# Performance work log

Measured on AMD Instinct MI355X. Metric: run time of the kernel, lower is better.

## Reference

```python
import jax, jax.numpy as jnp
import numpy as np

D_MODEL = 768
NUM_HEADS = 12
D_K = D_MODEL // NUM_HEADS


def setup_inputs() -> dict:
    key = jax.random.key(0)
    ks = jax.random.split(key, 11)
    B, S = 2, 2048
    s = 1.0 / np.sqrt(D_MODEL)
    inp = {
        'q': jax.random.normal(ks[0], (B, S, D_MODEL), jnp.float32),
        'k': jax.random.normal(ks[1], (B, S, D_MODEL), jnp.float32),
        'v': jax.random.normal(ks[2], (B, S, D_MODEL), jnp.float32),
        'w_q': jax.random.normal(ks[3], (D_MODEL, D_MODEL), jnp.float32) * s,
        'b_q': jnp.zeros((D_MODEL,), jnp.float32),
        'w_k': jax.random.normal(ks[4], (D_MODEL, D_MODEL), jnp.float32) * s,
        'b_k': jnp.zeros((D_MODEL,), jnp.float32),
        'w_v': jax.random.normal(ks[5], (D_MODEL, D_MODEL), jnp.float32) * s,
        'b_v': jnp.zeros((D_MODEL,), jnp.float32),
        'w_o': jax.random.normal(ks[6], (D_MODEL, D_MODEL), jnp.float32) * s,
        'b_o': jnp.zeros((D_MODEL,), jnp.float32),
    }
    return inp


def _split_heads(x):
    # (B, S, D) -> (B, H, S, d_k)
    B, S, _ = x.shape
    return x.reshape(B, S, NUM_HEADS, D_K).transpose(0, 2, 1, 3)


def reference(q, k, v, w_q, b_q, w_k, b_k, w_v, b_v, w_o, b_o):
    qh = _split_heads(q @ w_q + b_q)
    kh = _split_heads(k @ w_k + b_k)
    vh = _split_heads(v @ w_v + b_v)
    scale = 1.0 / jnp.sqrt(jnp.asarray(D_K, qh.dtype))
    scores = jnp.einsum('bhqd,bhkd->bhqk', qh, kh) * scale  # [B,H,Sq,Sk]
    attn_weights = jax.nn.softmax(scores, axis=-1)
    ctx = jnp.einsum('bhqk,bhkd->bhqd', attn_weights, vh)
    B, H, S, _ = ctx.shape
    ctx = ctx.transpose(0, 2, 1, 3).reshape(B, S, D_MODEL)
    out = ctx @ w_o + b_o  # dropout = identity (eval mode)
    return out, attn_weights
```

## Files before the change

### kernel.cpp

```cpp
#include <hip/hip_runtime.h>
#include <math.h>

#define HH 12
#define SS 2048
#define DM 768
#define DK 64

typedef _Float16 f16x8 __attribute__((ext_vector_type(8)));
typedef _Float16 f16x4 __attribute__((ext_vector_type(4)));
typedef float    f32x4 __attribute__((ext_vector_type(4)));

#define MFMA_F16(A, B, C) __builtin_amdgcn_mfma_f32_16x16x32_f16((A), (B), (C), 0, 0, 0)

template <int MODE>
__global__ __launch_bounds__(256) void gemm_bias_kernel(
        const float* __restrict__ A, const float* __restrict__ W,
        const float* __restrict__ bias, float* __restrict__ C,
        _Float16* __restrict__ Chi, _Float16* __restrict__ Clo)
{
    __shared__ float Ast[16][68];
    __shared__ float Bs[16][68];

    const int tid = threadIdx.x;
    const int tx = tid & 15, ty = tid >> 4;
    const int n0 = blockIdx.x * 64;
    const int m0 = blockIdx.y * 64;

    float acc[4][4] = {};

    for (int kt = 0; kt < 48; ++kt) {
        __syncthreads();
        #pragma unroll
        for (int it = 0; it < 4; ++it) {
            int idx = tid + it * 256;
            int r = idx >> 4, c = idx & 15;
            Ast[c][r] = A[(size_t)(m0 + r) * DM + kt * 16 + c];
        }
        {
            int r = tid >> 4, c = tid & 15;
            *(float4*)&Bs[r][c << 2] =
                *(const float4*)&W[(size_t)(kt * 16 + r) * DM + n0 + (c << 2)];
        }
        __syncthreads();

        #pragma unroll 4
        for (int kk = 0; kk < 16; ++kk) {
            float4 a4 = *(const float4*)&Ast[kk][ty << 2];
            float4 b4 = *(const float4*)&Bs[kk][tx << 2];
            float av[4] = {a4.x, a4.y, a4.z, a4.w};
            float bv[4] = {b4.x, b4.y, b4.z, b4.w};
            #pragma unroll
            for (int i = 0; i < 4; ++i)
                #pragma unroll
                for (int j = 0; j < 4; ++j)
                    acc[i][j] = fmaf(av[i], bv[j], acc[i][j]);
        }
    }

    const float4 bb4 = *(const float4*)&bias[n0 + (tx << 2)];
    const float bvv[4] = {bb4.x, bb4.y, bb4.z, bb4.w};

    if (MODE == 0) {
        #pragma unroll
        for (int i = 0; i < 4; ++i) {
            int m = m0 + ty * 4 + i;
            float4 o;
            o.x = acc[i][0] + bvv[0];
            o.y = acc[i][1] + bvv[1];
            o.z = acc[i][2] + bvv[2];
            o.w = acc[i][3] + bvv[3];
            *(float4*)&C[(size_t)m * DM + n0 + (tx << 2)] = o;
        }
    } else if (MODE == 1) {
        const int h = blockIdx.x;
        #pragma unroll
        for (int i = 0; i < 4; ++i) {
            int m = m0 + ty * 4 + i;
            int b_ = m >> 11, s_ = m & 2047;
            size_t base = (((size_t)(b_ * HH + h) * SS + s_) << 6) + (tx << 2);
            f16x4 hi, lo;
            #pragma unroll
            for (int j = 0; j < 4; ++j) {
                float v = acc[i][j] + bvv[j];
                _Float16 hv = (_Float16)v;
                hi[j] = hv;
                lo[j] = (_Float16)(v - (float)hv);
            }
            *(f16x4*)&Chi[base] = hi;
            *(f16x4*)&Clo[base] = lo;
        }
    } else {
        const int h  = blockIdx.x;
        const int m  = m0 + ty * 4;
        const int b_ = m >> 11;
        const int s_ = m & 2047;
        #pragma unroll
        for (int j = 0; j < 4; ++j) {
            int dk = (tx << 2) + j;
            size_t base = ((size_t)(b_ * HH + h) * DK + dk) * SS + s_;
            f16x4 hi, lo;
            #pragma unroll
            for (int i = 0; i < 4; ++i) {
                float v = acc[i][j] + bvv[j];
                _Float16 hv = (_Float16)v;
                hi[i] = hv;
                lo[i] = (_Float16)(v - (float)hv);
            }
            *(f16x4*)&Chi[base] = hi;
            *(f16x4*)&Clo[base] = lo;
        }
    }
}

__global__ __launch_bounds__(256) void attn_kernel(
        const _Float16* __restrict__ Qhi, const _Float16* __restrict__ Qlo,
        const _Float16* __restrict__ Khi, const _Float16* __restrict__ Klo,
        const _Float16* __restrict__ Vthi, const _Float16* __restrict__ Vtlo,
        float* __restrict__ attnW, float* __restrict__ ctx)
{
    __shared__ float Ps[4][16][34];

    const int tid  = threadIdx.x;
    const int wave = tid >> 6;
    const int lane = tid & 63;
    const int lrow = lane & 15;
    const int lk   = (lane >> 4) * 8;
    const int grow = (lane >> 4) * 4;

    const int qt = blockIdx.x;
    const int bh = blockIdx.y;
    const int qw0 = qt * 64 + wave * 16;
    const size_t qkbase = (size_t)bh * SS * DK;
    const size_t vbase  = (size_t)bh * DK * SS;

    f16x8 qhi[2], qlo[2];
    {
        const size_t qidx = qkbase + (size_t)(qw0 + lrow) * DK + lk;
        qhi[0] = *(const f16x8*)&Qhi[qidx];
        qhi[1] = *(const f16x8*)&Qhi[qidx + 32];
        qlo[0] = *(const f16x8*)&Qlo[qidx];
        qlo[1] = *(const f16x8*)&Qlo[qidx + 32];
    }

    float lsum[4] = {0.f, 0.f, 0.f, 0.f};
    #pragma unroll 2
    for (int kt = 0; kt < 128; ++kt) {
        const size_t kidx = qkbase + (size_t)(kt * 16 + lrow) * DK + lk;
        f16x8 khi0 = *(const f16x8*)&Khi[kidx];
        f16x8 khi1 = *(const f16x8*)&Khi[kidx + 32];
        f16x8 klo0 = *(const f16x8*)&Klo[kidx];
        f16x8 klo1 = *(const f16x8*)&Klo[kidx + 32];
        f32x4 acc = {0.f, 0.f, 0.f, 0.f};
        acc = MFMA_F16(qhi[0], khi0, acc);
        acc = MFMA_F16(qhi[1], khi1, acc);
        acc = MFMA_F16(qlo[0], khi0, acc);
        acc = MFMA_F16(qlo[1], khi1, acc);
        acc = MFMA_F16(qhi[0], klo0, acc);
        acc = MFMA_F16(qhi[1], klo1, acc);
        #pragma unroll
        for (int r = 0; r < 4; ++r)
            lsum[r] += __expf(acc[r] * 0.125f);
    }

    #pragma unroll
    for (int r = 0; r < 4; ++r) {
        lsum[r] += __shfl_xor(lsum[r], 1, 64);
        lsum[r] += __shfl_xor(lsum[r], 2, 64);
        lsum[r] += __shfl_xor(lsum[r], 4, 64);
        lsum[r] += __shfl_xor(lsum[r], 8, 64);
    }
    float rl[4];
    #pragma unroll
    for (int r = 0; r < 4; ++r) rl[r] = 1.0f / lsum[r];

    f32x4 Oacc[4];
    #pragma unroll
    for (int n = 0; n < 4; ++n) Oacc[n] = (f32x4){0.f, 0.f, 0.f, 0.f};

    float (*ps)[34] = Ps[wave];

    for (int kt = 0; kt < 64; ++kt) {
        #pragma unroll
        for (int sub = 0; sub < 2; ++sub) {
            const int k16 = kt * 2 + sub;
            const size_t kidx = qkbase + (size_t)(k16 * 16 + lrow) * DK + lk;
            f16x8 khi0 = *(const f16x8*)&Khi[kidx];
            f16x8 khi1 = *(const f16x8*)&Khi[kidx + 32];
            f16x8 klo0 = *(const f16x8*)&Klo[kidx];
            f16x8 klo1 = *(const f16x8*)&Klo[kidx + 32];
            f32x4 acc = {0.f, 0.f, 0.f, 0.f};
            acc = MFMA_F16(qhi[0], khi0, acc);
            acc = MFMA_F16(qhi[1], khi1, acc);
            acc = MFMA_F16(qlo[0], khi0, acc);
            acc = MFMA_F16(qlo[1], khi1, acc);
            acc = MFMA_F16(qhi[0], klo0, acc);
            acc = MFMA_F16(qhi[1], klo1, acc);
            #pragma unroll
            for (int r = 0; r < 4; ++r) {
                float p = __expf(acc[r] * 0.125f) * rl[r];
                attnW[((size_t)bh * SS + qw0 + grow + r) * SS + k16 * 16 + lrow] = p;
                ps[grow + r][sub * 16 + lrow] = p * 512.0f;
            }
        }
        float pf[8];
        #pragma unroll
        for (int j = 0; j < 8; ++j) pf[j] = ps[lrow][lk + j];
        f16x8 phi, plo;
        #pragma unroll
        for (int j = 0; j < 8; ++j) {
            _Float16 h = (_Float16)pf[j];
            phi[j] = h;
            plo[j] = (_Float16)(pf[j] - (float)h);
        }
        #pragma unroll
        for (int n = 0; n < 4; ++n) {
            const size_t vidx = vbase + (size_t)(n * 16 + lrow) * SS + kt * 32 + lk;
            f16x8 vhi = *(const f16x8*)&Vthi[vidx];
            f16x8 vlo = *(const f16x8*)&Vtlo[vidx];
            Oacc[n] = MFMA_F16(phi, vhi, Oacc[n]);
            Oacc[n] = MFMA_F16(plo, vhi, Oacc[n]);
            Oacc[n] = MFMA_F16(phi, vlo, Oacc[n]);
        }
    }

    const int b_ = bh / HH, h_ = bh % HH;
    #pragma unroll
    for (int n = 0; n < 4; ++n)
        #pragma unroll
        for (int r = 0; r < 4; ++r) {
            int q = qw0 + grow + r;
            ctx[((size_t)b_ * SS + q) * DM + h_ * DK + n * 16 + lrow] =
                Oacc[n][r] * 0.001953125f;
        }
}

extern "C" void kernel_launch(void* const* d_in, const int* in_sizes, int n_in,
                              void* d_out, int out_size, void* d_ws, size_t ws_size,
                              hipStream_t stream) {
    const float* q   = (const float*)d_in[0];
    const float* k   = (const float*)d_in[1];
    const float* v   = (const float*)d_in[2];
    const float* w_q = (const float*)d_in[3];
    const float* b_q = (const float*)d_in[4];
    const float* w_k = (const float*)d_in[5];
    const float* b_k = (const float*)d_in[6];
    const float* w_v = (const float*)d_in[7];
    const float* b_v = (const float*)d_in[8];
    const float* w_o = (const float*)d_in[9];
    const float* b_o = (const float*)d_in[10];

    float* out   = (float*)d_out;
    float* attnW = out + (size_t)2 * SS * DM;

    _Float16* wsh  = (_Float16*)d_ws;
    const size_t PL = (size_t)2 * HH * SS * DK;
    _Float16* Qhi  = wsh;
    _Float16* Qlo  = wsh + PL;
    _Float16* Khi  = wsh + 2 * PL;
    _Float16* Klo  = wsh + 3 * PL;
    _Float16* Vthi = wsh + 4 * PL;
    _Float16* Vtlo = wsh + 5 * PL;
    float* ctx     = (float*)(wsh + 6 * PL);

    dim3 gg(12, 64), blk(256);
    gemm_bias_kernel<1><<<gg, blk, 0, stream>>>(q, w_q, b_q, nullptr, Qhi, Qlo);
    gemm_bias_kernel<1><<<gg, blk, 0, stream>>>(k, w_k, b_k, nullptr, Khi, Klo);
    gemm_bias_kernel<2><<<gg, blk, 0, stream>>>(v, w_v, b_v, nullptr, Vthi, Vtlo);

    attn_kernel<<<dim3(32, 24), blk, 0, stream>>>(Qhi, Qlo, Khi, Klo, Vthi, Vtlo,
                                                  attnW, ctx);

    gemm_bias_kernel<0><<<gg, blk, 0, stream>>>(ctx, w_o, b_o, out, nullptr, nullptr);
}
```

Before: 1.236 ms.

## Use split-fp16 MFMA projection GEMMs and single-pass attention with deferred normalization

The fp32 FMA projection GEMMs are replaced by MFMA GEMMs on split hi/lo fp16 operands. Weights are pre-converted and transposed into scratch space inside the output buffers, and the V output is transposed through LDS so stores are coalesced. The attention kernel drops its separate row-sum pass. It writes unnormalized exp scores, then rescales the attention-weight rows afterwards and normalizes ctx by the row sum, trading the second QK^T recomputation for an extra read/write of attnW. Unnormalized exp without max subtraction risks overflow, and the output needs an extra copy kernel because the out buffer is reused as scratch.

New measurement: 1.317 ms. 6.5% more time.

```diff
diff --git a/kernel.cpp b/kernel.cpp
--- a/kernel.cpp
+++ b/kernel.cpp
@@ -12,103 +12,144 @@
 
 #define MFMA_F16(A, B, C) __builtin_amdgcn_mfma_f32_16x16x32_f16((A), (B), (C), 0, 0, 0)
 
+__global__ __launch_bounds__(256) void conv_w_kernel(
+        const float* __restrict__ w0, const float* __restrict__ w1,
+        const float* __restrict__ w2, const float* __restrict__ w3,
+        _Float16* hi0, _Float16* lo0, _Float16* hi1, _Float16* lo1,
+        _Float16* hi2, _Float16* lo2, _Float16* hi3, _Float16* lo3)
+{
+    __shared__ float T[64][68];
+    const int z = blockIdx.z;
+    const float* W = (z == 0) ? w0 : (z == 1) ? w1 : (z == 2) ? w2 : w3;
+    _Float16* Whi  = (z == 0) ? hi0 : (z == 1) ? hi1 : (z == 2) ? hi2 : hi3;
+    _Float16* Wlo  = (z == 0) ? lo0 : (z == 1) ? lo1 : (z == 2) ? lo2 : lo3;
+
+    const int tid = threadIdx.x;
+    const int k0 = blockIdx.y * 64, n0 = blockIdx.x * 64;
+
+    #pragma unroll
+    for (int i = 0; i < 4; ++i) {
+        int r = (tid >> 4) + i * 16;
+        int c = (tid & 15) * 4;
+        *(float4*)&T[r][c] = *(const float4*)&W[(size_t)(k0 + r) * DM + n0 + c];
+    }
+    __syncthreads();
+
+    const int n = tid >> 2, kq = (tid & 3) * 16;
+    f16x8 ha, la, hb, lb;
+    #pragma unroll
+    for (int j = 0; j < 8; ++j) {
+        float v = T[kq + j][n];
+        _Float16 h = (_Float16)v;
+        ha[j] = h; la[j] = (_Float16)(v - (float)h);
+    }
+    #pragma unroll
+    for (int j = 0; j < 8; ++j) {
+        float v = T[kq + 8 + j][n];
+        _Float16 h = (_Float16)v;
+        hb[j] = h; lb[j] = (_Float16)(v - (float)h);
+    }
+    size_t o = (size_t)(n0 + n) * DM + k0 + kq;
+    *(f16x8*)&Whi[o]     = ha;
+    *(f16x8*)&Whi[o + 8] = hb;
+    *(f16x8*)&Wlo[o]     = la;
+    *(f16x8*)&Wlo[o + 8] = lb;
+}
+
 template <int MODE>
-__global__ __launch_bounds__(256) void gemm_bias_kernel(
-        const float* __restrict__ A, const float* __restrict__ W,
-        const float* __restrict__ bias, float* __restrict__ C,
-        _Float16* __restrict__ Chi, _Float16* __restrict__ Clo)
+__global__ __launch_bounds__(256) void gemm16_kernel(
+        const float* __restrict__ A, const _Float16* __restrict__ Bhi,
+        const _Float16* __restrict__ Blo, const float* __restrict__ bias,
+        _Float16* __restrict__ Chi, _Float16* __restrict__ Clo,
+        float* __restrict__ Cf)
 {
-    __shared__ float Ast[16][68];
-    __shared__ float Bs[16][68];
-
-    const int tid = threadIdx.x;
-    const int tx = tid & 15, ty = tid >> 4;
-    const int n0 = blockIdx.x * 64;
-    const int m0 = blockIdx.y * 64;
-
-    float acc[4][4] = {};
-
-    for (int kt = 0; kt < 48; ++kt) {
+    const int tid  = threadIdx.x;
+    const int wave = tid >> 6, lane = tid & 63;
+    const int lrow = lane & 15;
+    const int lk   = (lane >> 4) * 8;
+    const int grow = (lane >> 4) * 4;
+    const int n0   = blockIdx.x * 64;
+    const int m0   = blockIdx.y * 64;
+    const int mr   = m0 + wave * 16 + lrow;
+
+    f32x4 acc[4];
+    #pragma unroll
+    for (int nf = 0; nf < 4; ++nf) acc[nf] = (f32x4){0.f, 0.f, 0.f, 0.f};
+
+    const float* Arow = A + (size_t)mr * DM;
+
+    #pragma unroll 2
+    for (int kt = 0; kt < 24; ++kt) {
+        const int k0 = kt * 32 + lk;
+        float4 x = *(const float4*)&Arow[k0];
+        float4 y = *(const float4*)&Arow[k0 + 4];
+        float vv[8] = {x.x, x.y, x.z, x.w, y.x, y.y, y.z, y.w};
+        f16x8 ah, al;
+        #pragma unroll
+        for (int j = 0; j < 8; ++j) {
+            _Float16 h = (_Float16)vv[j];
+            ah[j] = h; al[j] = (_Float16)(vv[j] - (float)h);
+        }
+        #pragma unroll
+        for (int nf = 0; nf < 4; ++nf) {
+            const size_t bo = (size_t)(n0 + nf * 16 + lrow) * DM + k0;
+            f16x8 bh_ = *(const f16x8*)&Bhi[bo];
+            f16x8 bl_ = *(const f16x8*)&Blo[bo];
+            acc[nf] = MFMA_F16(ah, bh_, acc[nf]);
+            acc[nf] = MFMA_F16(al, bh_, acc[nf]);
+            acc[nf] = MFMA_F16(ah, bl_, acc[nf]);
+        }
+    }
+
+    float bb[4];
+    #pragma unroll
+    for (int nf = 0; nf < 4; ++nf) bb[nf] = bias[n0 + nf * 16 + lrow];
+
+    if (MODE == 0) {
+        const int h = blockIdx.x;
+        #pragma unroll
+        for (int nf = 0; nf < 4; ++nf)
+            #pragma unroll
+            for (int r = 0; r < 4; ++r) {
+                int m = m0 + wave * 16 + grow + r;
+                int b_ = m >> 11, s_ = m & 2047;
+                float v = acc[nf][r] + bb[nf];
+                _Float16 h16 = (_Float16)v;
+                size_t o = (((size_t)(b_ * HH + h) * SS + s_) << 6) + nf * 16 + lrow;
+                Chi[o] = h16;
+                Clo[o] = (_Float16)(v - (float)h16);
+            }
+    } else if (MODE == 1) {
+        __shared__ _Float16 T[2][64][72];
+        #pragma unroll
+        for (int nf = 0; nf < 4; ++nf)
+            #pragma unroll
+            for (int r = 0; r < 4; ++r) {
+                float v = acc[nf][r] + bb[nf];
+                _Float16 h16 = (_Float16)v;
+                int ml = wave * 16 + grow + r;
+                T[0][nf * 16 + lrow][ml] = h16;
+                T[1][nf * 16 + lrow][ml] = (_Float16)(v - (float)h16);
+            }
         __syncthreads();
-        #pragma unroll
-        for (int it = 0; it < 4; ++it) {
-            int idx = tid + it * 256;
-            int r = idx >> 4, c = idx & 15;
-            Ast[c][r] = A[(size_t)(m0 + r) * DM + kt * 16 + c];
-        }
-        {
-            int r = tid >> 4, c = tid & 15;
-            *(float4*)&Bs[r][c << 2] =
-                *(const float4*)&W[(size_t)(kt * 16 + r) * DM + n0 + (c << 2)];
-        }
-        __syncthreads();
-
-        #pragma unroll 4
-        for (int kk = 0; kk < 16; ++kk) {
-            float4 a4 = *(const float4*)&Ast[kk][ty << 2];
-            float4 b4 = *(const float4*)&Bs[kk][tx << 2];
-            float av[4] = {a4.x, a4.y, a4.z, a4.w};
-            float bv[4] = {b4.x, b4.y, b4.z, b4.w};
+        const int h  = blockIdx.x;
+        const int b_ = m0 >> 11, s0 = m0 & 2047;
+        int row = tid >> 1;
+        int p = row >> 6, dk = row & 63, sh = (tid & 1) * 32;
+        const _Float16* src = &T[p][dk][sh];
+        _Float16* dst = (p ? Clo : Chi) +
+                        ((size_t)(b_ * HH + h) * DK + dk) * SS + s0 + sh;
+        #pragma unroll
+        for (int j = 0; j < 32; j += 8)
+            *(f16x8*)&dst[j] = *(const f16x8*)&src[j];
+    } else {
+        #pragma unroll
+        for (int nf = 0; nf < 4; ++nf)
             #pragma unroll
-            for (int i = 0; i < 4; ++i)
-                #pragma unroll
-                for (int j = 0; j < 4; ++j)
-                    acc[i][j] = fmaf(av[i], bv[j], acc[i][j]);
-        }
-    }
-
-    const float4 bb4 = *(const float4*)&bias[n0 + (tx << 2)];
-    const float bvv[4] = {bb4.x, bb4.y, bb4.z, bb4.w};
-
-    if (MODE == 0) {
-        #pragma unroll
-        for (int i = 0; i < 4; ++i) {
-            int m = m0 + ty * 4 + i;
-            float4 o;
-            o.x = acc[i][0] + bvv[0];
-            o.y = acc[i][1] + bvv[1];
-            o.z = acc[i][2] + bvv[2];
-            o.w = acc[i][3] + bvv[3];
-            *(float4*)&C[(size_t)m * DM + n0 + (tx << 2)] = o;
-        }
-    } else if (MODE == 1) {
-        const int h = blockIdx.x;
-        #pragma unroll
-        for (int i = 0; i < 4; ++i) {
-            int m = m0 + ty * 4 + i;
-            int b_ = m >> 11, s_ = m & 2047;
-            size_t base = (((size_t)(b_ * HH + h) * SS + s_) << 6) + (tx << 2);
-            f16x4 hi, lo;
-            #pragma unroll
-            for (int j = 0; j < 4; ++j) {
-                float v = acc[i][j] + bvv[j];
-                _Float16 hv = (_Float16)v;
-                hi[j] = hv;
-                lo[j] = (_Float16)(v - (float)hv);
+            for (int r = 0; r < 4; ++r) {
+                int m = m0 + wave * 16 + grow + r;
+                Cf[(size_t)m * DM + n0 + nf * 16 + lrow] = acc[nf][r] + bb[nf];
             }
-            *(f16x4*)&Chi[base] = hi;
-            *(f16x4*)&Clo[base] = lo;
-        }
-    } else {
-        const int h  = blockIdx.x;
-        const int m  = m0 + ty * 4;
-        const int b_ = m >> 11;
-        const int s_ = m & 2047;
-        #pragma unroll
-        for (int j = 0; j < 4; ++j) {
-            int dk = (tx << 2) + j;
-            size_t base = ((size_t)(b_ * HH + h) * DK + dk) * SS + s_;
-            f16x4 hi, lo;
-            #pragma unroll
-            for (int i = 0; i < 4; ++i) {
-                float v = acc[i][j] + bvv[j];
-                _Float16 hv = (_Float16)v;
-                hi[i] = hv;
-                lo[i] = (_Float16)(v - (float)hv);
-            }
-            *(f16x4*)&Chi[base] = hi;
-            *(f16x4*)&Clo[base] = lo;
-        }
     }
 }
 
@@ -143,36 +184,6 @@
     }
 
     float lsum[4] = {0.f, 0.f, 0.f, 0.f};
-    #pragma unroll 2
-    for (int kt = 0; kt < 128; ++kt) {
-        const size_t kidx = qkbase + (size_t)(kt * 16 + lrow) * DK + lk;
-        f16x8 khi0 = *(const f16x8*)&Khi[kidx];
-        f16x8 khi1 = *(const f16x8*)&Khi[kidx + 32];
-        f16x8 klo0 = *(const f16x8*)&Klo[kidx];
-        f16x8 klo1 = *(const f16x8*)&Klo[kidx + 32];
-        f32x4 acc = {0.f, 0.f, 0.f, 0.f};
-        acc = MFMA_F16(qhi[0], khi0, acc);
-        acc = MFMA_F16(qhi[1], khi1, acc);
-        acc = MFMA_F16(qlo[0], khi0, acc);
-        acc = MFMA_F16(qlo[1], khi1, acc);
-        acc = MFMA_F16(qhi[0], klo0, acc);
-        acc = MFMA_F16(qhi[1], klo1, acc);
-        #pragma unroll
-        for (int r = 0; r < 4; ++r)
-            lsum[r] += __expf(acc[r] * 0.125f);
-    }
-
-    #pragma unroll
-    for (int r = 0; r < 4; ++r) {
-        lsum[r] += __shfl_xor(lsum[r], 1, 64);
-        lsum[r] += __shfl_xor(lsum[r], 2, 64);
-        lsum[r] += __shfl_xor(lsum[r], 4, 64);
-        lsum[r] += __shfl_xor(lsum[r], 8, 64);
-    }
-    float rl[4];
-    #pragma unroll
-    for (int r = 0; r < 4; ++r) rl[r] = 1.0f / lsum[r];
-
     f32x4 Oacc[4];
     #pragma unroll
     for (int n = 0; n < 4; ++n) Oacc[n] = (f32x4){0.f, 0.f, 0.f, 0.f};
@@ -188,18 +199,20 @@
             f16x8 khi1 = *(const f16x8*)&Khi[kidx + 32];
             f16x8 klo0 = *(const f16x8*)&Klo[kidx];
             f16x8 klo1 = *(const f16x8*)&Klo[kidx + 32];
-            f32x4 acc = {0.f, 0.f, 0.f, 0.f};
-            acc = MFMA_F16(qhi[0], khi0, acc);
-            acc = MFMA_F16(qhi[1], khi1, acc);
-            acc = MFMA_F16(qlo[0], khi0, acc);
-            acc = MFMA_F16(qlo[1], khi1, acc);
-            acc = MFMA_F16(qhi[0], klo0, acc);
-            acc = MFMA_F16(qhi[1], klo1, acc);
+            f32x4 cA = {0.f, 0.f, 0.f, 0.f};
+            f32x4 cB = {0.f, 0.f, 0.f, 0.f};
+            cA = MFMA_F16(qhi[0], khi0, cA);
+            cA = MFMA_F16(qhi[1], khi1, cA);
+            cA = MFMA_F16(qlo[0], khi0, cA);
+            cB = MFMA_F16(qlo[1], khi1, cB);
+            cB = MFMA_F16(qhi[0], klo0, cB);
+            cB = MFMA_F16(qhi[1], klo1, cB);
             #pragma unroll
             for (int r = 0; r < 4; ++r) {
-                float p = __expf(acc[r] * 0.125f) * rl[r];
-                attnW[((size_t)bh * SS + qw0 + grow + r) * SS + k16 * 16 + lrow] = p;
-                ps[grow + r][sub * 16 + lrow] = p * 512.0f;
+                float pv = __expf((cA[r] + cB[r]) * 0.125f);
+                lsum[r] += pv;
+                attnW[((size_t)bh * SS + qw0 + grow + r) * SS + k16 * 16 + lrow] = pv;
+                ps[grow + r][sub * 16 + lrow] = pv * 16.0f;
             }
         }
         float pf[8];
@@ -223,6 +236,33 @@
         }
     }
 
+    #pragma unroll
+    for (int r = 0; r < 4; ++r) {
+        lsum[r] += __shfl_xor(lsum[r], 1, 64);
+        lsum[r] += __shfl_xor(lsum[r], 2, 64);
+        lsum[r] += __shfl_xor(lsum[r], 4, 64);
+        lsum[r] += __shfl_xor(lsum[r], 8, 64);
+    }
+    float rl[4];
+    #pragma unroll
+    for (int r = 0; r < 4; ++r) rl[r] = 1.0f / lsum[r];
+
+    if (lrow == 0) {
+        #pragma unroll
+        for (int r = 0; r < 4; ++r) ps[grow + r][32] = rl[r];
+    }
+
+    for (int r16 = 0; r16 < 16; ++r16) {
+        float mrl = ps[r16][32];
+        float4* row4 = (float4*)&attnW[((size_t)bh * SS + qw0 + r16) * SS];
+        #pragma unroll
+        for (int it = 0; it < 8; ++it) {
+            float4 vv = row4[it * 64 + lane];
+            vv.x *= mrl; vv.y *= mrl; vv.z *= mrl; vv.w *= mrl;
+            row4[it * 64 + lane] = vv;
+        }
+    }
+
     const int b_ = bh / HH, h_ = bh % HH;
     #pragma unroll
     for (int n = 0; n < 4; ++n)
@@ -230,8 +270,19 @@
         for (int r = 0; r < 4; ++r) {
             int q = qw0 + grow + r;
             ctx[((size_t)b_ * SS + q) * DM + h_ * DK + n * 16 + lrow] =
-                Oacc[n][r] * 0.001953125f;
-        }
+                Oacc[n][r] * rl[r] * 0.0625f;
+        }
+}
+
+__global__ __launch_bounds__(256) void copy_kernel(
+        float* __restrict__ dst, const float* __restrict__ src)
+{
+    const size_t total4 = (size_t)2 * SS * DM / 4;
+    size_t i = (size_t)blockIdx.x * 256 + threadIdx.x;
+    const size_t stride = (size_t)gridDim.x * 256;
+    float4* d4 = (float4*)dst;
+    const float4* s4 = (const float4*)src;
+    for (; i < total4; i += stride) d4[i] = s4[i];
 }
 
 extern "C" void kernel_launch(void* const* d_in, const int* in_sizes, int n_in,
@@ -252,7 +303,7 @@
     float* out   = (float*)d_out;
     float* attnW = out + (size_t)2 * SS * DM;
 
-    _Float16* wsh  = (_Float16*)d_ws;
+    _Float16* wsh = (_Float16*)d_ws;
     const size_t PL = (size_t)2 * HH * SS * DK;
     _Float16* Qhi  = wsh;
     _Float16* Qlo  = wsh + PL;
@@ -260,15 +311,34 @@
     _Float16* Klo  = wsh + 3 * PL;
     _Float16* Vthi = wsh + 4 * PL;
     _Float16* Vtlo = wsh + 5 * PL;
-    float* ctx     = (float*)(wsh + 6 * PL);
-
-    dim3 gg(12, 64), blk(256);
-    gemm_bias_kernel<1><<<gg, blk, 0, stream>>>(q, w_q, b_q, nullptr, Qhi, Qlo);
-    gemm_bias_kernel<1><<<gg, blk, 0, stream>>>(k, w_k, b_k, nullptr, Khi, Klo);
-    gemm_bias_kernel<2><<<gg, blk, 0, stream>>>(v, w_v, b_v, nullptr, Vthi, Vtlo);
+    float* ctx = (float*)(wsh + 6 * PL);
+    float* res = (float*)wsh;
+
+    const size_t WPL = (size_t)DM * DM;
+    _Float16* WtQ_hi = (_Float16*)attnW;
+    _Float16* WtQ_lo = WtQ_hi + WPL;
+    _Float16* WtK_hi = WtQ_hi + 2 * WPL;
+    _Float16* WtK_lo = WtQ_hi + 3 * WPL;
+    _Float16* WtV_hi = WtQ_hi + 4 * WPL;
+    _Float16* WtV_lo = WtQ_hi + 5 * WPL;
+    _Float16* WtO_hi = (_Float16*)out;
+    _Float16* WtO_lo = WtO_hi + WPL;
+
+    dim3 blk(256);
+    conv_w_kernel<<<dim3(12, 12, 4), blk, 0, stream>>>(
+        w_q, w_k, w_v, w_o,
+        WtQ_hi, WtQ_lo, WtK_hi, WtK_lo, WtV_hi, WtV_lo, WtO_hi, WtO_lo);
+
+    dim3 gg(12, 64);
+    gemm16_kernel<0><<<gg, blk, 0, stream>>>(q, WtQ_hi, WtQ_lo, b_q, Qhi, Qlo, nullptr);
+    gemm16_kernel<0><<<gg, blk, 0, stream>>>(k, WtK_hi, WtK_lo, b_k, Khi, Klo, nullptr);
+    gemm16_kernel<1><<<gg, blk, 0, stream>>>(v, WtV_hi, WtV_lo, b_v, Vthi, Vtlo, nullptr);
 
     attn_kernel<<<dim3(32, 24), blk, 0, stream>>>(Qhi, Qlo, Khi, Klo, Vthi, Vtlo,
                                                   attnW, ctx);
 
-    gemm_bias_kernel<0><<<gg, blk, 0, stream>>>(ctx, w_o, b_o, out, nullptr, nullptr);
-}
+    gemm16_kernel<2><<<gg, blk, 0, stream>>>(ctx, WtO_hi, WtO_lo, b_o,
+                                             nullptr, nullptr, res);
+
+    copy_kernel<<<dim3(1024), blk, 0, stream>>>(out, res);
+}
```
